# Optimization experiments

Measured on AMD Instinct MI355X. Metric: run time of the kernel, lower is better.

Reference implementation:

```python
import jax, jax.numpy as jnp
import numpy as np

EMBED = 256
HEADS = 8
LEVELS = 3
POINTS = 4
MLP = 4
SS = np.array([[100, 100], [50, 50], [25, 25]], np.int32)  # (H, W) per level


def setup_inputs() -> dict:
    key = jax.random.key(0)
    ks = jax.random.split(key, 12)
    B, Q = 2, 128 * 128
    NV = int((SS[:, 0] * SS[:, 1]).sum())
    C = EMBED
    F = C * MLP
    s = 0.02

    def w(k, shape):
        return jax.random.normal(k, shape, jnp.float32) * s

    return dict(
        query=jax.random.normal(ks[0], (B, Q, C), jnp.float32),
        value=jax.random.normal(ks[1], (B, NV, C), jnp.float32),
        query_pos=jax.random.normal(ks[2], (B, Q, C), jnp.float32),
        ref_pts=jax.random.uniform(ks[3], (B, Q, 2), jnp.float32),
        spatial_shapes=SS,
        level_start_index=np.concatenate([[0], np.cumsum(SS[:, 0] * SS[:, 1])[:-1]]).astype(np.int32),
        ln1_g=jnp.ones(C), ln1_b=jnp.zeros(C),
        ln2_g=jnp.ones(C), ln2_b=jnp.zeros(C),
        W_value=w(ks[4], (C, C)), b_value=jnp.zeros(C),
        W_off=w(ks[5], (C, HEADS * LEVELS * POINTS * 2)), b_off=w(ks[6], (HEADS * LEVELS * POINTS * 2,)),
        W_attn=w(ks[7], (C, HEADS * LEVELS * POINTS)), b_attn=jnp.zeros(HEADS * LEVELS * POINTS),
        W_out=w(ks[8], (C, C)), b_out=jnp.zeros(C),
        W_ffn1=w(ks[9], (C, F)), b_ffn1=jnp.zeros(F),
        W_ffn2=w(ks[10], (F, C)), b_ffn2=jnp.zeros(C),
    )


def _layernorm(x, g, b, eps=1e-5):
    m = x.mean(-1, keepdims=True)
    v = ((x - m) ** 2).mean(-1, keepdims=True)
    return (x - m) * jax.lax.rsqrt(v + eps) * g + b


def _bilinear(v, loc, Hl, Wl):
    # v: [BH, Hl*Wl, d]; loc: [BH, Q, P, 2] normalized to [0,1].
    # grid_sample(align_corners=False, padding=zeros): pixel = loc*size - 0.5
    BH, Q, P, _ = loc.shape
    d = v.shape[-1]
    x = loc[..., 0] * Wl - 0.5
    y = loc[..., 1] * Hl - 0.5
    x0f = jnp.floor(x)
    y0f = jnp.floor(y)
    lx = x - x0f
    ly = y - y0f
    x0 = x0f.astype(jnp.int32)
    y0 = y0f.astype(jnp.int32)

    def gather(xi, yi):
        valid = ((xi >= 0) & (xi < Wl) & (yi >= 0) & (yi < Hl)).astype(v.dtype)
        idx = jnp.clip(yi, 0, Hl - 1) * Wl + jnp.clip(xi, 0, Wl - 1)
        g = jnp.take_along_axis(v, idx.reshape(BH, Q * P, 1), axis=1).reshape(BH, Q, P, d)
        return g * valid[..., None]

    w00 = (1 - lx) * (1 - ly)
    w01 = lx * (1 - ly)
    w10 = (1 - lx) * ly
    w11 = lx * ly
    return (gather(x0, y0) * w00[..., None] + gather(x0 + 1, y0) * w01[..., None]
            + gather(x0, y0 + 1) * w10[..., None] + gather(x0 + 1, y0 + 1) * w11[..., None])


def _forward(query, value, query_pos, ref_pts, spatial_shapes,
             ln1_g, ln1_b, ln2_g, ln2_b,
             W_value, b_value, W_off, b_off, W_attn, b_attn, W_out, b_out,
             W_ffn1, b_ffn1, W_ffn2, b_ffn2):
    B, Q, C = query.shape
    Hh, L, P = HEADS, LEVELS, POINTS
    d = C // Hh
    ss = np.asarray(spatial_shapes)
    starts = np.concatenate([[0], np.cumsum(ss[:, 0] * ss[:, 1])])

    # pre-norm + positional embedding (MSDeformAttn adds query_pos)
    qn = _layernorm(query, ln1_g, ln1_b)
    q = qn + query_pos

    # value projection, split heads
    v = (value @ W_value + b_value).reshape(B, -1, Hh, d)

    off = (q @ W_off + b_off).reshape(B, Q, Hh, L, P, 2)
    aw = jax.nn.softmax((q @ W_attn + b_attn).reshape(B, Q, Hh, L * P), axis=-1)
    aw = aw.reshape(B, Q, Hh, L, P)

    # offset normalizer is (W, H) per level
    normalizer = jnp.asarray(ss[:, ::-1].copy(), jnp.float32)
    # bev_value path: ref_pts broadcast over levels
    loc = ref_pts[:, :, None, None, None, :] + off / normalizer[None, None, None, :, None, :]

    out = jnp.zeros((B * Hh, Q, d), query.dtype)
    for l in range(L):
        Hl, Wl = int(ss[l, 0]), int(ss[l, 1])
        v_l = v[:, starts[l]:starts[l + 1]].transpose(0, 2, 1, 3).reshape(B * Hh, Hl * Wl, d)
        loc_l = loc[:, :, :, l].transpose(0, 2, 1, 3, 4).reshape(B * Hh, Q, P, 2)
        sampled = _bilinear(v_l, loc_l, Hl, Wl)  # [BH, Q, P, d]
        w_l = aw[:, :, :, l].transpose(0, 2, 1, 3).reshape(B * Hh, Q, P)
        out = out + (sampled * w_l[..., None]).sum(2)

    out = out.reshape(B, Hh, Q, d).transpose(0, 2, 1, 3).reshape(B, Q, C)
    x = query + (out @ W_out + b_out)

    h = _layernorm(x, ln2_g, ln2_b)
    x = x + (jax.nn.gelu(h @ W_ffn1 + b_ffn1, approximate=False) @ W_ffn2 + b_ffn2)
    return x


def reference(query, value, query_pos, ref_pts, spatial_shapes, level_start_index,
              ln1_g, ln1_b, ln2_g, ln2_b,
              W_value, b_value, W_off, b_off, W_attn, b_attn, W_out, b_out,
              W_ffn1, b_ffn1, W_ffn2, b_ffn2):
    return _forward(query, value, query_pos, ref_pts, spatial_shapes,
                    ln1_g, ln1_b, ln2_g, ln2_b,
                    W_value, b_value, W_off, b_off, W_attn, b_attn, W_out, b_out,
                    W_ffn1, b_ffn1, W_ffn2, b_ffn2)
```

## Files before the change

### kernel.cpp

```cpp
#include <hip/hip_runtime.h>
#include <hip/hip_bf16.h>

#define BQ      2
#define QLEN    16384
#define CDIM    256
#define HEADS   8
#define LEV     3
#define PTS     4
#define DHEAD   32
#define NVTOT   13125
#define FDIM    1024
#define NTOK    (BQ*QLEN)
#define MROWS_V (BQ*NVTOT)
#define NPROJ   288

typedef __attribute__((ext_vector_type(8))) short short8;
typedef __attribute__((ext_vector_type(4))) float floatx4;

typedef const __attribute__((address_space(1))) unsigned int gu32;
typedef __attribute__((address_space(3))) unsigned int lu32;

struct bf16x4 { __hip_bfloat16 v[4]; };

__device__ __forceinline__ int imin(int a, int b){ return a<b?a:b; }
__device__ __forceinline__ int imax(int a, int b){ return a>b?a:b; }

__device__ __forceinline__ float bf2f(unsigned short u){ return __uint_as_float((unsigned)u << 16); }
__device__ __forceinline__ unsigned short f2bf(float f)
{
    __hip_bfloat16 h = __float2bfloat16(f);
    return *(unsigned short*)&h;
}
__device__ __forceinline__ unsigned long long pack4(float4 v)
{
    unsigned long long r = (unsigned long long)f2bf(v.x)
                         | ((unsigned long long)f2bf(v.y) << 16)
                         | ((unsigned long long)f2bf(v.z) << 32)
                         | ((unsigned long long)f2bf(v.w) << 48);
    return r;
}
__device__ __forceinline__ float4 unpack4(unsigned long long c)
{
    float4 v;
    v.x = bf2f((unsigned short)(c));
    v.y = bf2f((unsigned short)(c >> 16));
    v.z = bf2f((unsigned short)(c >> 32));
    v.w = bf2f((unsigned short)(c >> 48));
    return v;
}

__device__ __forceinline__ float gelu_f(float x)
{
    float u = 0.7978845608028654f * (x + 0.044715f * x * x * x);
    float e = __expf(2.0f * u);
    float th = 1.0f - 2.0f / (e + 1.0f);
    return 0.5f * x * (1.0f + th);
}

__global__ __launch_bounds__(256)
void ln_bf16_k(const float* __restrict__ x, const float* __restrict__ pos,
               const float* __restrict__ g, const float* __restrict__ b,
               __hip_bfloat16* __restrict__ out)
{
    int tok  = blockIdx.x * 4 + (threadIdx.x >> 6);
    int lane = threadIdx.x & 63;
    float4 v = ((const float4*)(x + (size_t)tok * CDIM))[lane];
    float s = v.x + v.y + v.z + v.w;
    #pragma unroll
    for (int o = 32; o > 0; o >>= 1) s += __shfl_down(s, o);
    s = __shfl(s, 0);
    float mean = s * (1.0f / 256.0f);
    float4 c; c.x = v.x - mean; c.y = v.y - mean; c.z = v.z - mean; c.w = v.w - mean;
    float q2 = c.x*c.x + c.y*c.y + c.z*c.z + c.w*c.w;
    #pragma unroll
    for (int o = 32; o > 0; o >>= 1) q2 += __shfl_down(q2, o);
    q2 = __shfl(q2, 0);
    float rstd = rsqrtf(q2 * (1.0f / 256.0f) + 1e-5f);
    float4 gg = ((const float4*)g)[lane];
    float4 bb = ((const float4*)b)[lane];
    float4 o4;
    o4.x = c.x * rstd * gg.x + bb.x;
    o4.y = c.y * rstd * gg.y + bb.y;
    o4.z = c.z * rstd * gg.z + bb.z;
    o4.w = c.w * rstd * gg.w + bb.w;
    if (pos) {
        float4 p = ((const float4*)(pos + (size_t)tok * CDIM))[lane];
        o4.x += p.x; o4.y += p.y; o4.z += p.z; o4.w += p.w;
    }
    *(unsigned long long*)(out + (size_t)tok * CDIM + lane * 4) = pack4(o4);
}

__global__ __launch_bounds__(256)
void cvt_k(const float* __restrict__ in, __hip_bfloat16* __restrict__ out, int n4)
{
    int i = blockIdx.x * 256 + threadIdx.x;
    if (i >= n4) return;
    float4 v = ((const float4*)in)[i];
    *(unsigned long long*)(out + (size_t)i * 4) = pack4(v);
}

__global__ __launch_bounds__(256)
void wt_all_k(const float* __restrict__ Wv,  const float* __restrict__ Woff,
              const float* __restrict__ Wat, const float* __restrict__ Wout,
              const float* __restrict__ W1,  const float* __restrict__ W2,
              const float* __restrict__ boff, const float* __restrict__ bat,
              __hip_bfloat16* __restrict__ o_v,  __hip_bfloat16* __restrict__ o_c,
              __hip_bfloat16* __restrict__ o_out,
              __hip_bfloat16* __restrict__ o_1,  __hip_bfloat16* __restrict__ o_2,
              float* __restrict__ o_bc)
{
    int gid = blockIdx.x * 256 + threadIdx.x;
    if (gid < 65536) {
        int idx = gid, n = idx >> 8, k = idx & 255;
        o_v[idx] = __float2bfloat16(Wv[(size_t)k * 256 + n]);
    } else if (gid < 163840) {
        int idx = gid - 65536, n = idx >> 8, k = idx & 255;
        float v = 0.0f;
        if (n < 192)       v = Woff[(size_t)k * 192 + n];
        else if (n < 288)  v = Wat[(size_t)k * 96 + (n - 192)];
        o_c[idx] = __float2bfloat16(v);
    } else if (gid < 229376) {
        int idx = gid - 163840, n = idx >> 8, k = idx & 255;
        o_out[idx] = __float2bfloat16(Wout[(size_t)k * 256 + n]);
    } else if (gid < 491520) {
        int idx = gid - 229376, n = idx >> 8, k = idx & 255;
        o_1[idx] = __float2bfloat16(W1[(size_t)k * 1024 + n]);
    } else if (gid < 753664) {
        int idx = gid - 491520, n = idx >> 10, k = idx & 1023;
        o_2[idx] = __float2bfloat16(W2[(size_t)k * 256 + n]);
    } else if (gid < 753952) {
        int idx = gid - 753664;
        o_bc[idx] = (idx < 192) ? boff[idx] : bat[idx - 192];
    }
}

enum { EP_PLAIN_BF16 = 0, EP_VSCAT_BF16 = 1, EP_RES = 2, EP_GELU_BF16 = 3 };

__global__ __launch_bounds__(256)
void mm_k(const __hip_bfloat16* __restrict__ A, const __hip_bfloat16* __restrict__ Bt,
          const float* __restrict__ bias, const float* __restrict__ res,
          void* __restrict__ Cout, int M, int N, int K, int mode)
{
    __shared__ float4 smem4[2048];
    __hip_bfloat16* Ws = (__hip_bfloat16*)smem4;
    __hip_bfloat16* Ts = (__hip_bfloat16*)smem4 + 128*64;
    unsigned long long* st = (unsigned long long*)smem4;
    int t = threadIdx.x;
    int lane = t & 63;
    int wave = t >> 6;
    int wm = wave >> 1, wn = wave & 1;
    int lm = lane & 15, lk = lane >> 4;
    int m0 = blockIdx.x * 128;
    int n0 = blockIdx.y * 128;

    floatx4 acc[4][4];
    #pragma unroll
    for (int i = 0; i < 4; i++)
        #pragma unroll
        for (int j = 0; j < 4; j++) acc[i][j] = (floatx4)0.0f;

    for (int kt = 0; kt < K; kt += 64) {
        #pragma unroll
        for (int i = 0; i < 4; i++) {
            int cc  = i * 256 + t;
            int row = cc >> 3;
            int c   = cc & 7;
            int kc  = c ^ (row & 7);
            int ra  = m0 + row; if (ra >= M) ra = M - 1;
            const __hip_bfloat16* gw = Bt + (size_t)(n0 + row) * K + kt + kc * 8;
            const __hip_bfloat16* gt = A  + (size_t)ra * K + kt + kc * 8;
            __builtin_amdgcn_global_load_lds((gu32*)gw, (lu32*)(Ws + cc * 8), 16, 0, 0);
            __builtin_amdgcn_global_load_lds((gu32*)gt, (lu32*)(Ts + cc * 8), 16, 0, 0);
        }
        __syncthreads();
        #pragma unroll
        for (int ks = 0; ks < 2; ks++) {
            short8 wf[4], tf[4];
            #pragma unroll
            for (int i = 0; i < 4; i++) {
                int rw = wn * 64 + i * 16 + lm;
                int cw = (ks * 4 + lk) ^ (rw & 7);
                wf[i] = *(const short8*)(Ws + (rw * 8 + cw) * 8);
                int rt = wm * 64 + i * 16 + lm;
                int ct = (ks * 4 + lk) ^ (rt & 7);
                tf[i] = *(const short8*)(Ts + (rt * 8 + ct) * 8);
            }
            #pragma unroll
            for (int i = 0; i < 4; i++)
                #pragma unroll
                for (int j = 0; j < 4; j++)
                    acc[i][j] = __builtin_amdgcn_mfma_f32_16x16x32_bf16(wf[i], tf[j], acc[i][j], 0, 0, 0);
        }
        __syncthreads();
    }

    #pragma unroll
    for (int i = 0; i < 4; i++) {
        int chan = n0 + wn * 64 + i * 16 + lk * 4;
        float4 b4 = make_float4(0.f, 0.f, 0.f, 0.f);
        if (chan < N) b4 = *(const float4*)(bias + chan);
        int c4 = wn * 16 + i * 4 + lk;
        #pragma unroll
        for (int j = 0; j < 4; j++) {
            int tl = wm * 64 + j * 16 + lm;
            float4 v;
            v.x = acc[i][j][0] + b4.x;
            v.y = acc[i][j][1] + b4.y;
            v.z = acc[i][j][2] + b4.z;
            v.w = acc[i][j][3] + b4.w;
            st[tl * 32 + (c4 ^ (tl & 31))] = pack4(v);
        }
    }
    __syncthreads();

    int rel  = (t & 31) * 4;
    int c4r  = t & 31;
    #pragma unroll
    for (int it = 0; it < 16; it++) {
        int tl   = it * 8 + (t >> 5);
        int tok  = m0 + tl;
        int chan = n0 + rel;
        if (tok >= M || chan >= N) continue;
        unsigned long long chunk = st[tl * 32 + (c4r ^ (tl & 31))];
        if (mode == EP_PLAIN_BF16) {
            *(unsigned long long*)((__hip_bfloat16*)Cout + (size_t)tok * N + chan) = chunk;
        } else if (mode == EP_VSCAT_BF16) {
            int bb  = tok / NVTOT;
            int pix = tok - bb * NVTOT;
            int hd  = chan >> 5, dc = chan & 31;
            *(unsigned long long*)((__hip_bfloat16*)Cout
                + (((size_t)(bb * HEADS + hd)) * NVTOT + pix) * DHEAD + dc) = chunk;
        } else if (mode == EP_GELU_BF16) {
            float4 v = unpack4(chunk);
            v.x = gelu_f(v.x); v.y = gelu_f(v.y); v.z = gelu_f(v.z); v.w = gelu_f(v.w);
            *(unsigned long long*)((__hip_bfloat16*)Cout + (size_t)tok * N + chan) = pack4(v);
        } else {
            float4 v = unpack4(chunk);
            float4 rr = *(const float4*)(res + (size_t)tok * N + chan);
            v.x += rr.x; v.y += rr.y; v.z += rr.z; v.w += rr.w;
            *(float4*)((float*)Cout + (size_t)tok * N + chan) = v;
        }
    }
}

__global__ __launch_bounds__(256)
void sample_k(const __hip_bfloat16* __restrict__ v, const __hip_bfloat16* __restrict__ cbuf,
              const float* __restrict__ ref, __hip_bfloat16* __restrict__ out)
{
    __shared__ int4   metaIdx[4 * 104];
    __shared__ float4 metaW[4 * 104];

    int wid  = threadIdx.x >> 6;
    int lane = threadIdx.x & 63;
    int t    = blockIdx.x * 4 + wid;
    int b    = t >> 14;
    float rx = ref[(size_t)t * 2 + 0];
    float ry = ref[(size_t)t * 2 + 1];
    const __hip_bfloat16* crow = cbuf + (size_t)t * NPROJ;

    #pragma unroll
    for (int rnd = 0; rnd < 2; rnd++) {
        int slot = rnd * 64 + lane;
        int h = slot >> 4, p = slot & 15;
        int pc = imin(p, 11);
        unsigned upk = *(const unsigned*)(crow + h * 24 + pc * 2);
        float ox = bf2f((unsigned short)upk);
        float oy = bf2f((unsigned short)(upk >> 16));
        float logit = bf2f(*(const unsigned short*)(crow + 192 + h * 12 + pc));
        float mx = logit;
        #pragma unroll
        for (int o = 8; o > 0; o >>= 1) mx = fmaxf(mx, __shfl_xor(mx, o, 16));
        float e = (p < 12) ? __expf(logit - mx) : 0.0f;
        float ssum = e;
        #pragma unroll
        for (int o = 8; o > 0; o >>= 1) ssum += __shfl_xor(ssum, o, 16);
        float aw = e / ssum;

        if (p < 12) {
            int l = p >> 2;
            float fS = (l == 0) ? 100.0f : ((l == 1) ? 50.0f : 25.0f);
            int   Wl = (l == 0) ? 100 : ((l == 1) ? 50 : 25);
            int   st = (l == 0) ? 0 : ((l == 1) ? 10000 : 12500);
            float x = (rx + ox / fS) * fS - 0.5f;
            float y = (ry + oy / fS) * fS - 0.5f;
            float x0f = floorf(x), y0f = floorf(y);
            float fx = x - x0f, fy = y - y0f;
            int x0 = (int)x0f, y0 = (int)y0f;
            int x1 = x0 + 1,  y1 = y0 + 1;
            int cx0 = imin(imax(x0, 0), Wl - 1), cx1 = imin(imax(x1, 0), Wl - 1);
            int cy0 = imin(imax(y0, 0), Wl - 1), cy1 = imin(imax(y1, 0), Wl - 1);
            float vx0 = (x0 >= 0 && x0 < Wl) ? 1.0f : 0.0f;
            float vx1 = (x1 >= 0 && x1 < Wl) ? 1.0f : 0.0f;
            float vy0 = (y0 >= 0 && y0 < Wl) ? 1.0f : 0.0f;
            float vy1 = (y1 >= 0 && y1 < Wl) ? 1.0f : 0.0f;
            int s = wid * 104 + h * 13 + p;
            metaIdx[s] = make_int4(st + cy0 * Wl + cx0, st + cy0 * Wl + cx1,
                                   st + cy1 * Wl + cx0, st + cy1 * Wl + cx1);
            metaW[s] = make_float4((1.0f - fx) * (1.0f - fy) * aw * vx0 * vy0,
                                   fx * (1.0f - fy) * aw * vx1 * vy0,
                                   (1.0f - fx) * fy * aw * vx0 * vy1,
                                   fx * fy * aw * vx1 * vy1);
        }
    }
    __syncthreads();

    int h  = lane >> 3;
    int c8 = lane & 7;
    const __hip_bfloat16* vbh = v + ((size_t)(b * HEADS + h)) * NVTOT * DHEAD + c8 * 4;
    float4 acc = {0.0f, 0.0f, 0.0f, 0.0f};
    #pragma unroll
    for (int p = 0; p < 12; p++) {
        int s = wid * 104 + h * 13 + p;
        int4   mi = metaIdx[s];
        float4 mw = metaW[s];
        ushort4 r0 = *(const ushort4*)(vbh + (size_t)mi.x * DHEAD);
        ushort4 r1 = *(const ushort4*)(vbh + (size_t)mi.y * DHEAD);
        ushort4 r2 = *(const ushort4*)(vbh + (size_t)mi.z * DHEAD);
        ushort4 r3 = *(const ushort4*)(vbh + (size_t)mi.w * DHEAD);
        acc.x = fmaf(mw.x, bf2f(r0.x), acc.x);
        acc.y = fmaf(mw.x, bf2f(r0.y), acc.y);
        acc.z = fmaf(mw.x, bf2f(r0.z), acc.z);
        acc.w = fmaf(mw.x, bf2f(r0.w), acc.w);
        acc.x = fmaf(mw.y, bf2f(r1.x), acc.x);
        acc.y = fmaf(mw.y, bf2f(r1.y), acc.y);
        acc.z = fmaf(mw.y, bf2f(r1.z), acc.z);
        acc.w = fmaf(mw.y, bf2f(r1.w), acc.w);
        acc.x = fmaf(mw.z, bf2f(r2.x), acc.x);
        acc.y = fmaf(mw.z, bf2f(r2.y), acc.y);
        acc.z = fmaf(mw.z, bf2f(r2.z), acc.z);
        acc.w = fmaf(mw.z, bf2f(r2.w), acc.w);
        acc.x = fmaf(mw.w, bf2f(r3.x), acc.x);
        acc.y = fmaf(mw.w, bf2f(r3.y), acc.y);
        acc.z = fmaf(mw.w, bf2f(r3.z), acc.z);
        acc.w = fmaf(mw.w, bf2f(r3.w), acc.w);
    }
    *(unsigned long long*)(out + (size_t)t * CDIM + h * DHEAD + c8 * 4) = pack4(acc);
}

extern "C" void kernel_launch(void* const* d_in, const int* in_sizes, int n_in,
                              void* d_out, int out_size, void* d_ws, size_t ws_size,
                              hipStream_t stream)
{
    const float* query = (const float*)d_in[0];
    const float* value = (const float*)d_in[1];
    const float* qpos  = (const float*)d_in[2];
    const float* ref   = (const float*)d_in[3];
    const float* ln1g  = (const float*)d_in[6];
    const float* ln1b  = (const float*)d_in[7];
    const float* ln2g  = (const float*)d_in[8];
    const float* ln2b  = (const float*)d_in[9];
    const float* Wv    = (const float*)d_in[10];
    const float* bv    = (const float*)d_in[11];
    const float* Woff  = (const float*)d_in[12];
    const float* boff  = (const float*)d_in[13];
    const float* Wat   = (const float*)d_in[14];
    const float* bat   = (const float*)d_in[15];
    const float* Wout  = (const float*)d_in[16];
    const float* bout  = (const float*)d_in[17];
    const float* W1    = (const float*)d_in[18];
    const float* b1    = (const float*)d_in[19];
    const float* W2    = (const float*)d_in[20];
    const float* b2    = (const float*)d_in[21];
    float* out = (float*)d_out;
    char*  ws  = (char*)d_ws;

    const size_t MB = 1024 * 1024;
    __hip_bfloat16* Wvt   = (__hip_bfloat16*)(ws + 0);
    __hip_bfloat16* Wct   = (__hip_bfloat16*)(ws + 131072);
    __hip_bfloat16* Woutt = (__hip_bfloat16*)(ws + 327680);
    __hip_bfloat16* W1t   = (__hip_bfloat16*)(ws + 458752);
    __hip_bfloat16* W2t   = (__hip_bfloat16*)(ws + 983040);
    float*          bcomb = (float*)(ws + 1507328);
    __hip_bfloat16* qbf   = (__hip_bfloat16*)(ws + 2  * MB);
    __hip_bfloat16* aoutb = (__hip_bfloat16*)(ws + 19 * MB);
    __hip_bfloat16* vbf   = (__hip_bfloat16*)(ws + 36 * MB);
    __hip_bfloat16* vbuf  = (__hip_bfloat16*)(ws + 50 * MB);
    __hip_bfloat16* cbuf  = (__hip_bfloat16*)(ws + 77 * MB);
    __hip_bfloat16* gbf   = (__hip_bfloat16*)(ws + 100 * MB);
    __hip_bfloat16* hbf   = qbf;

    wt_all_k<<<2946, 256, 0, stream>>>(Wv, Woff, Wat, Wout, W1, W2, boff, bat,
                                       Wvt, Wct, Woutt, W1t, W2t, bcomb);
    cvt_k<<<(MROWS_V * CDIM / 4 + 255) / 256, 256, 0, stream>>>(value, vbf, MROWS_V * CDIM / 4);
    ln_bf16_k<<<NTOK / 4, 256, 0, stream>>>(query, qpos, ln1g, ln1b, qbf);
    mm_k<<<dim3((MROWS_V + 127) / 128, 2), 256, 0, stream>>>(
        vbf, Wvt, bv, nullptr, vbuf, MROWS_V, 256, 256, EP_VSCAT_BF16);
    mm_k<<<dim3(NTOK / 128, 3), 256, 0, stream>>>(
        qbf, Wct, bcomb, nullptr, cbuf, NTOK, NPROJ, 256, EP_PLAIN_BF16);
    sample_k<<<NTOK / 4, 256, 0, stream>>>(vbuf, cbuf, ref, aoutb);
    mm_k<<<dim3(NTOK / 128, 2), 256, 0, stream>>>(
        aoutb, Woutt, bout, query, out, NTOK, 256, 256, EP_RES);
    ln_bf16_k<<<NTOK / 4, 256, 0, stream>>>(out, nullptr, ln2g, ln2b, hbf);
    mm_k<<<dim3(NTOK / 128, 8), 256, 0, stream>>>(
        hbf, W1t, b1, nullptr, gbf, NTOK, FDIM, 256, EP_GELU_BF16);
    mm_k<<<dim3(NTOK / 128, 2), 256, 0, stream>>>(
        gbf, W2t, b2, out, out, NTOK, 256, FDIM, EP_RES);
}
```

Baseline: 367.6 us.

## Fuse prep kernels, keep residual in bf16, token-major value layout, cheaper gelu/sampling math

Merges the weight transpose, value conversion and first layernorm into one launch. The intermediate residual stream is now stored as bf16 instead of fp32 and read back in bf16 by the second layernorm and the final GEMM epilogue. The value projection writes plain token-major output, and the sampler gathers 8-byte chunks using pre-shifted byte offsets. GELU uses a sigmoid-form tanh approximation with a hardware reciprocal, and the sample coordinate math is simplified. Together these cut memory traffic and launches, at the cost of extra bf16 rounding on the residual path.

```diff
diff --git a/kernel.cpp b/kernel.cpp
--- a/kernel.cpp
+++ b/kernel.cpp
@@ -16,12 +16,11 @@
 
 typedef __attribute__((ext_vector_type(8))) short short8;
 typedef __attribute__((ext_vector_type(4))) float floatx4;
+typedef unsigned long long u64;
 
 typedef const __attribute__((address_space(1))) unsigned int gu32;
 typedef __attribute__((address_space(3))) unsigned int lu32;
 
-struct bf16x4 { __hip_bfloat16 v[4]; };
-
 __device__ __forceinline__ int imin(int a, int b){ return a<b?a:b; }
 __device__ __forceinline__ int imax(int a, int b){ return a>b?a:b; }
 
@@ -31,15 +30,12 @@
     __hip_bfloat16 h = __float2bfloat16(f);
     return *(unsigned short*)&h;
 }
-__device__ __forceinline__ unsigned long long pack4(float4 v)
-{
-    unsigned long long r = (unsigned long long)f2bf(v.x)
-                         | ((unsigned long long)f2bf(v.y) << 16)
-                         | ((unsigned long long)f2bf(v.z) << 32)
-                         | ((unsigned long long)f2bf(v.w) << 48);
-    return r;
-}
-__device__ __forceinline__ float4 unpack4(unsigned long long c)
+__device__ __forceinline__ u64 pack4(float4 v)
+{
+    return (u64)f2bf(v.x) | ((u64)f2bf(v.y) << 16)
+         | ((u64)f2bf(v.z) << 32) | ((u64)f2bf(v.w) << 48);
+}
+__device__ __forceinline__ float4 unpack4(u64 c)
 {
     float4 v;
     v.x = bf2f((unsigned short)(c));
@@ -51,20 +47,17 @@
 
 __device__ __forceinline__ float gelu_f(float x)
 {
-    float u = 0.7978845608028654f * (x + 0.044715f * x * x * x);
-    float e = __expf(2.0f * u);
-    float th = 1.0f - 2.0f / (e + 1.0f);
-    return 0.5f * x * (1.0f + th);
-}
-
-__global__ __launch_bounds__(256)
-void ln_bf16_k(const float* __restrict__ x, const float* __restrict__ pos,
-               const float* __restrict__ g, const float* __restrict__ b,
-               __hip_bfloat16* __restrict__ out)
-{
-    int tok  = blockIdx.x * 4 + (threadIdx.x >> 6);
-    int lane = threadIdx.x & 63;
-    float4 v = ((const float4*)(x + (size_t)tok * CDIM))[lane];
+    float u2 = x * x;
+    float a  = x * fmaf(0.0713548163f, u2, 1.5957691216f);
+    float e  = __expf(a);
+    float r  = __builtin_amdgcn_rcpf(e + 1.0f);
+    return fmaf(-x, r, x);
+}
+
+__device__ __forceinline__ void ln_core(float4 v, const float* __restrict__ pos, int tok,
+                                        const float* __restrict__ g, const float* __restrict__ b,
+                                        int lane, __hip_bfloat16* __restrict__ out)
+{
     float s = v.x + v.y + v.z + v.w;
     #pragma unroll
     for (int o = 32; o > 0; o >>= 1) s += __shfl_down(s, o);
@@ -87,64 +80,87 @@
         float4 p = ((const float4*)(pos + (size_t)tok * CDIM))[lane];
         o4.x += p.x; o4.y += p.y; o4.z += p.z; o4.w += p.w;
     }
-    *(unsigned long long*)(out + (size_t)tok * CDIM + lane * 4) = pack4(o4);
-}
+    *(u64*)(out + (size_t)tok * CDIM + lane * 4) = pack4(o4);
+}
+
+#define WT_BLOCKS  2946
+#define CVT_BLOCKS 6563
+#define LN_BLOCKS  8192
 
 __global__ __launch_bounds__(256)
-void cvt_k(const float* __restrict__ in, __hip_bfloat16* __restrict__ out, int n4)
-{
-    int i = blockIdx.x * 256 + threadIdx.x;
-    if (i >= n4) return;
-    float4 v = ((const float4*)in)[i];
-    *(unsigned long long*)(out + (size_t)i * 4) = pack4(v);
+void prep_k(const float* __restrict__ Wv,  const float* __restrict__ Woff,
+            const float* __restrict__ Wat, const float* __restrict__ Wout,
+            const float* __restrict__ W1,  const float* __restrict__ W2,
+            const float* __restrict__ boff, const float* __restrict__ bat,
+            const float* __restrict__ value, const float* __restrict__ query,
+            const float* __restrict__ qpos,  const float* __restrict__ ln1g,
+            const float* __restrict__ ln1b,
+            __hip_bfloat16* __restrict__ o_v,  __hip_bfloat16* __restrict__ o_c,
+            __hip_bfloat16* __restrict__ o_out,
+            __hip_bfloat16* __restrict__ o_1,  __hip_bfloat16* __restrict__ o_2,
+            float* __restrict__ o_bc,
+            __hip_bfloat16* __restrict__ vbf,  __hip_bfloat16* __restrict__ qbf)
+{
+    int bx = blockIdx.x;
+    if (bx < WT_BLOCKS) {
+        int gid = bx * 256 + threadIdx.x;
+        if (gid < 65536) {
+            int idx = gid, n = idx >> 8, k = idx & 255;
+            o_v[idx] = __float2bfloat16(Wv[(size_t)k * 256 + n]);
+        } else if (gid < 163840) {
+            int idx = gid - 65536, n = idx >> 8, k = idx & 255;
+            float v = 0.0f;
+            if (n < 192)       v = Woff[(size_t)k * 192 + n];
+            else if (n < 288)  v = Wat[(size_t)k * 96 + (n - 192)];
+            o_c[idx] = __float2bfloat16(v);
+        } else if (gid < 229376) {
+            int idx = gid - 163840, n = idx >> 8, k = idx & 255;
+            o_out[idx] = __float2bfloat16(Wout[(size_t)k * 256 + n]);
+        } else if (gid < 491520) {
+            int idx = gid - 229376, n = idx >> 8, k = idx & 255;
+            o_1[idx] = __float2bfloat16(W1[(size_t)k * 1024 + n]);
+        } else if (gid < 753664) {
+            int idx = gid - 491520, n = idx >> 10, k = idx & 1023;
+            o_2[idx] = __float2bfloat16(W2[(size_t)k * 256 + n]);
+        } else if (gid < 753952) {
+            int idx = gid - 753664;
+            o_bc[idx] = (idx < 192) ? boff[idx] : bat[idx - 192];
+        }
+    } else if (bx < WT_BLOCKS + CVT_BLOCKS) {
+        int i = (bx - WT_BLOCKS) * 256 + threadIdx.x;
+        if (i < MROWS_V * CDIM / 4) {
+            float4 v = ((const float4*)value)[i];
+            *(u64*)(vbf + (size_t)i * 4) = pack4(v);
+        }
+    } else {
+        int tok  = (bx - WT_BLOCKS - CVT_BLOCKS) * 4 + (threadIdx.x >> 6);
+        int lane = threadIdx.x & 63;
+        float4 v = ((const float4*)(query + (size_t)tok * CDIM))[lane];
+        ln_core(v, qpos, tok, ln1g, ln1b, lane, qbf);
+    }
 }
 
 __global__ __launch_bounds__(256)
-void wt_all_k(const float* __restrict__ Wv,  const float* __restrict__ Woff,
-              const float* __restrict__ Wat, const float* __restrict__ Wout,
-              const float* __restrict__ W1,  const float* __restrict__ W2,
-              const float* __restrict__ boff, const float* __restrict__ bat,
-              __hip_bfloat16* __restrict__ o_v,  __hip_bfloat16* __restrict__ o_c,
-              __hip_bfloat16* __restrict__ o_out,
-              __hip_bfloat16* __restrict__ o_1,  __hip_bfloat16* __restrict__ o_2,
-              float* __restrict__ o_bc)
-{
-    int gid = blockIdx.x * 256 + threadIdx.x;
-    if (gid < 65536) {
-        int idx = gid, n = idx >> 8, k = idx & 255;
-        o_v[idx] = __float2bfloat16(Wv[(size_t)k * 256 + n]);
-    } else if (gid < 163840) {
-        int idx = gid - 65536, n = idx >> 8, k = idx & 255;
-        float v = 0.0f;
-        if (n < 192)       v = Woff[(size_t)k * 192 + n];
-        else if (n < 288)  v = Wat[(size_t)k * 96 + (n - 192)];
-        o_c[idx] = __float2bfloat16(v);
-    } else if (gid < 229376) {
-        int idx = gid - 163840, n = idx >> 8, k = idx & 255;
-        o_out[idx] = __float2bfloat16(Wout[(size_t)k * 256 + n]);
-    } else if (gid < 491520) {
-        int idx = gid - 229376, n = idx >> 8, k = idx & 255;
-        o_1[idx] = __float2bfloat16(W1[(size_t)k * 1024 + n]);
-    } else if (gid < 753664) {
-        int idx = gid - 491520, n = idx >> 10, k = idx & 1023;
-        o_2[idx] = __float2bfloat16(W2[(size_t)k * 256 + n]);
-    } else if (gid < 753952) {
-        int idx = gid - 753664;
-        o_bc[idx] = (idx < 192) ? boff[idx] : bat[idx - 192];
-    }
-}
-
-enum { EP_PLAIN_BF16 = 0, EP_VSCAT_BF16 = 1, EP_RES = 2, EP_GELU_BF16 = 3 };
+void ln2_k(const __hip_bfloat16* __restrict__ x, const float* __restrict__ g,
+           const float* __restrict__ b, __hip_bfloat16* __restrict__ out)
+{
+    int tok  = blockIdx.x * 4 + (threadIdx.x >> 6);
+    int lane = threadIdx.x & 63;
+    float4 v = unpack4(((const u64*)(x + (size_t)tok * CDIM))[lane]);
+    ln_core(v, nullptr, tok, g, b, lane, out);
+}
+
+enum { EP_PLAIN_BF16 = 0, EP_GELU_BF16 = 1, EP_RES_F2BF = 2, EP_RES_BF2F = 3 };
 
 __global__ __launch_bounds__(256)
 void mm_k(const __hip_bfloat16* __restrict__ A, const __hip_bfloat16* __restrict__ Bt,
-          const float* __restrict__ bias, const float* __restrict__ res,
+          const float* __restrict__ bias, const void* __restrict__ res,
           void* __restrict__ Cout, int M, int N, int K, int mode)
 {
     __shared__ float4 smem4[2048];
     __hip_bfloat16* Ws = (__hip_bfloat16*)smem4;
     __hip_bfloat16* Ts = (__hip_bfloat16*)smem4 + 128*64;
-    unsigned long long* st = (unsigned long long*)smem4;
+    u64* st = (u64*)smem4;
     int t = threadIdx.x;
     int lane = t & 63;
     int wave = t >> 6;
@@ -213,30 +229,29 @@
     }
     __syncthreads();
 
-    int rel  = (t & 31) * 4;
-    int c4r  = t & 31;
+    int rel = (t & 31) * 4;
+    int c4r = t & 31;
     #pragma unroll
     for (int it = 0; it < 16; it++) {
         int tl   = it * 8 + (t >> 5);
         int tok  = m0 + tl;
         int chan = n0 + rel;
         if (tok >= M || chan >= N) continue;
-        unsigned long long chunk = st[tl * 32 + (c4r ^ (tl & 31))];
+        u64 chunk = st[tl * 32 + (c4r ^ (tl & 31))];
         if (mode == EP_PLAIN_BF16) {
-            *(unsigned long long*)((__hip_bfloat16*)Cout + (size_t)tok * N + chan) = chunk;
-        } else if (mode == EP_VSCAT_BF16) {
-            int bb  = tok / NVTOT;
-            int pix = tok - bb * NVTOT;
-            int hd  = chan >> 5, dc = chan & 31;
-            *(unsigned long long*)((__hip_bfloat16*)Cout
-                + (((size_t)(bb * HEADS + hd)) * NVTOT + pix) * DHEAD + dc) = chunk;
+            *(u64*)((__hip_bfloat16*)Cout + (size_t)tok * N + chan) = chunk;
         } else if (mode == EP_GELU_BF16) {
             float4 v = unpack4(chunk);
             v.x = gelu_f(v.x); v.y = gelu_f(v.y); v.z = gelu_f(v.z); v.w = gelu_f(v.w);
-            *(unsigned long long*)((__hip_bfloat16*)Cout + (size_t)tok * N + chan) = pack4(v);
+            *(u64*)((__hip_bfloat16*)Cout + (size_t)tok * N + chan) = pack4(v);
+        } else if (mode == EP_RES_F2BF) {
+            float4 v = unpack4(chunk);
+            float4 rr = *(const float4*)((const float*)res + (size_t)tok * N + chan);
+            v.x += rr.x; v.y += rr.y; v.z += rr.z; v.w += rr.w;
+            *(u64*)((__hip_bfloat16*)Cout + (size_t)tok * N + chan) = pack4(v);
         } else {
             float4 v = unpack4(chunk);
-            float4 rr = *(const float4*)(res + (size_t)tok * N + chan);
+            float4 rr = unpack4(*(const u64*)((const __hip_bfloat16*)res + (size_t)tok * N + chan));
             v.x += rr.x; v.y += rr.y; v.z += rr.z; v.w += rr.w;
             *(float4*)((float*)Cout + (size_t)tok * N + chan) = v;
         }
@@ -274,15 +289,15 @@
         float ssum = e;
         #pragma unroll
         for (int o = 8; o > 0; o >>= 1) ssum += __shfl_xor(ssum, o, 16);
-        float aw = e / ssum;
+        float aw = e * __builtin_amdgcn_rcpf(ssum);
 
         if (p < 12) {
             int l = p >> 2;
             float fS = (l == 0) ? 100.0f : ((l == 1) ? 50.0f : 25.0f);
             int   Wl = (l == 0) ? 100 : ((l == 1) ? 50 : 25);
             int   st = (l == 0) ? 0 : ((l == 1) ? 10000 : 12500);
-            float x = (rx + ox / fS) * fS - 0.5f;
-            float y = (ry + oy / fS) * fS - 0.5f;
+            float x = fmaf(rx, fS, ox) - 0.5f;
+            float y = fmaf(ry, fS, oy) - 0.5f;
             float x0f = floorf(x), y0f = floorf(y);
             float fx = x - x0f, fy = y - y0f;
             int x0 = (int)x0f, y0 = (int)y0f;
@@ -294,8 +309,8 @@
             float vy0 = (y0 >= 0 && y0 < Wl) ? 1.0f : 0.0f;
             float vy1 = (y1 >= 0 && y1 < Wl) ? 1.0f : 0.0f;
             int s = wid * 104 + h * 13 + p;
-            metaIdx[s] = make_int4(st + cy0 * Wl + cx0, st + cy0 * Wl + cx1,
-                                   st + cy1 * Wl + cx0, st + cy1 * Wl + cx1);
+            metaIdx[s] = make_int4((st + cy0 * Wl + cx0) << 9, (st + cy0 * Wl + cx1) << 9,
+                                   (st + cy1 * Wl + cx0) << 9, (st + cy1 * Wl + cx1) << 9);
             metaW[s] = make_float4((1.0f - fx) * (1.0f - fy) * aw * vx0 * vy0,
                                    fx * (1.0f - fy) * aw * vx1 * vy0,
                                    (1.0f - fx) * fy * aw * vx0 * vy1,
@@ -305,36 +320,49 @@
     __syncthreads();
 
     int h  = lane >> 3;
-    int c8 = lane & 7;
-    const __hip_bfloat16* vbh = v + ((size_t)(b * HEADS + h)) * NVTOT * DHEAD + c8 * 4;
+    int bs = __builtin_amdgcn_readfirstlane(b);
+    const char* vb = (const char*)(v + (size_t)bs * NVTOT * CDIM);
+    int hoff = lane * 8;
     float4 acc = {0.0f, 0.0f, 0.0f, 0.0f};
     #pragma unroll
     for (int p = 0; p < 12; p++) {
         int s = wid * 104 + h * 13 + p;
         int4   mi = metaIdx[s];
         float4 mw = metaW[s];
-        ushort4 r0 = *(const ushort4*)(vbh + (size_t)mi.x * DHEAD);
-        ushort4 r1 = *(const ushort4*)(vbh + (size_t)mi.y * DHEAD);
-        ushort4 r2 = *(const ushort4*)(vbh + (size_t)mi.z * DHEAD);
-        ushort4 r3 = *(const ushort4*)(vbh + (size_t)mi.w * DHEAD);
-        acc.x = fmaf(mw.x, bf2f(r0.x), acc.x);
-        acc.y = fmaf(mw.x, bf2f(r0.y), acc.y);
-        acc.z = fmaf(mw.x, bf2f(r0.z), acc.z);
-        acc.w = fmaf(mw.x, bf2f(r0.w), acc.w);
-        acc.x = fmaf(mw.y, bf2f(r1.x), acc.x);
-        acc.y = fmaf(mw.y, bf2f(r1.y), acc.y);
-        acc.z = fmaf(mw.y, bf2f(r1.z), acc.z);
-        acc.w = fmaf(mw.y, bf2f(r1.w), acc.w);
-        acc.x = fmaf(mw.z, bf2f(r2.x), acc.x);
-        acc.y = fmaf(mw.z, bf2f(r2.y), acc.y);
-        acc.z = fmaf(mw.z, bf2f(r2.z), acc.z);
-        acc.w = fmaf(mw.z, bf2f(r2.w), acc.w);
-        acc.x = fmaf(mw.w, bf2f(r3.x), acc.x);
-        acc.y = fmaf(mw.w, bf2f(r3.y), acc.y);
-        acc.z = fmaf(mw.w, bf2f(r3.z), acc.z);
-        acc.w = fmaf(mw.w, bf2f(r3.w), acc.w);
-    }
-    *(unsigned long long*)(out + (size_t)t * CDIM + h * DHEAD + c8 * 4) = pack4(acc);
+        u64 g0 = *(const u64*)(vb + (unsigned)(mi.x + hoff));
+        u64 g1 = *(const u64*)(vb + (unsigned)(mi.y + hoff));
+        u64 g2 = *(const u64*)(vb + (unsigned)(mi.z + hoff));
+        u64 g3 = *(const u64*)(vb + (unsigned)(mi.w + hoff));
+        {
+            unsigned d0 = (unsigned)g0, d1 = (unsigned)(g0 >> 32);
+            acc.x = fmaf(mw.x, __uint_as_float(d0 << 16), acc.x);
+            acc.y = fmaf(mw.x, __uint_as_float(d0 & 0xffff0000u), acc.y);
+            acc.z = fmaf(mw.x, __uint_as_float(d1 << 16), acc.z);
+            acc.w = fmaf(mw.x, __uint_as_float(d1 & 0xffff0000u), acc.w);
+        }
+        {
+            unsigned d0 = (unsigned)g1, d1 = (unsigned)(g1 >> 32);
+            acc.x = fmaf(mw.y, __uint_as_float(d0 << 16), acc.x);
+            acc.y = fmaf(mw.y, __uint_as_float(d0 & 0xffff0000u), acc.y);
+            acc.z = fmaf(mw.y, __uint_as_float(d1 << 16), acc.z);
+            acc.w = fmaf(mw.y, __uint_as_float(d1 & 0xffff0000u), acc.w);
+        }
+        {
+            unsigned d0 = (unsigned)g2, d1 = (unsigned)(g2 >> 32);
+            acc.x = fmaf(mw.z, __uint_as_float(d0 << 16), acc.x);
+            acc.y = fmaf(mw.z, __uint_as_float(d0 & 0xffff0000u), acc.y);
+            acc.z = fmaf(mw.z, __uint_as_float(d1 << 16), acc.z);
+            acc.w = fmaf(mw.z, __uint_as_float(d1 & 0xffff0000u), acc.w);
+        }
+        {
+            unsigned d0 = (unsigned)g3, d1 = (unsigned)(g3 >> 32);
+            acc.x = fmaf(mw.w, __uint_as_float(d0 << 16), acc.x);
+            acc.y = fmaf(mw.w, __uint_as_float(d0 & 0xffff0000u), acc.y);
+            acc.z = fmaf(mw.w, __uint_as_float(d1 << 16), acc.z);
+            acc.w = fmaf(mw.w, __uint_as_float(d1 & 0xffff0000u), acc.w);
+        }
+    }
+    *(u64*)(out + (size_t)t * CDIM + lane * 4) = pack4(acc);
 }
 
 extern "C" void kernel_launch(void* const* d_in, const int* in_sizes, int n_in,
@@ -375,24 +403,24 @@
     __hip_bfloat16* aoutb = (__hip_bfloat16*)(ws + 19 * MB);
     __hip_bfloat16* vbf   = (__hip_bfloat16*)(ws + 36 * MB);
     __hip_bfloat16* vbuf  = (__hip_bfloat16*)(ws + 50 * MB);
-    __hip_bfloat16* cbuf  = (__hip_bfloat16*)(ws + 77 * MB);
+    __hip_bfloat16* xbf   = (__hip_bfloat16*)(ws + 64 * MB);
+    __hip_bfloat16* cbuf  = (__hip_bfloat16*)(ws + 81 * MB);
     __hip_bfloat16* gbf   = (__hip_bfloat16*)(ws + 100 * MB);
     __hip_bfloat16* hbf   = qbf;
 
-    wt_all_k<<<2946, 256, 0, stream>>>(Wv, Woff, Wat, Wout, W1, W2, boff, bat,
-                                       Wvt, Wct, Woutt, W1t, W2t, bcomb);
-    cvt_k<<<(MROWS_V * CDIM / 4 + 255) / 256, 256, 0, stream>>>(value, vbf, MROWS_V * CDIM / 4);
-    ln_bf16_k<<<NTOK / 4, 256, 0, stream>>>(query, qpos, ln1g, ln1b, qbf);
+    prep_k<<<WT_BLOCKS + CVT_BLOCKS + LN_BLOCKS, 256, 0, stream>>>(
+        Wv, Woff, Wat, Wout, W1, W2, boff, bat, value, query, qpos, ln1g, ln1b,
+        Wvt, Wct, Woutt, W1t, W2t, bcomb, vbf, qbf);
     mm_k<<<dim3((MROWS_V + 127) / 128, 2), 256, 0, stream>>>(
-        vbf, Wvt, bv, nullptr, vbuf, MROWS_V, 256, 256, EP_VSCAT_BF16);
+        vbf, Wvt, bv, nullptr, vbuf, MROWS_V, 256, 256, EP_PLAIN_BF16);
     mm_k<<<dim3(NTOK / 128, 3), 256, 0, stream>>>(
         qbf, Wct, bcomb, nullptr, cbuf, NTOK, NPROJ, 256, EP_PLAIN_BF16);
     sample_k<<<NTOK / 4, 256, 0, stream>>>(vbuf, cbuf, ref, aoutb);
     mm_k<<<dim3(NTOK / 128, 2), 256, 0, stream>>>(
-        aoutb, Woutt, bout, query, out, NTOK, 256, 256, EP_RES);
-    ln_bf16_k<<<NTOK / 4, 256, 0, stream>>>(out, nullptr, ln2g, ln2b, hbf);
+        aoutb, Woutt, bout, query, xbf, NTOK, 256, 256, EP_RES_F2BF);
+    ln2_k<<<NTOK / 4, 256, 0, stream>>>(xbf, ln2g, ln2b, hbf);
     mm_k<<<dim3(NTOK / 128, 8), 256, 0, stream>>>(
         hbf, W1t, b1, nullptr, gbf, NTOK, FDIM, 256, EP_GELU_BF16);
     mm_k<<<dim3(NTOK / 128, 2), 256, 0, stream>>>(
-        gbf, W2t, b2, out, out, NTOK, 256, FDIM, EP_RES);
-}
+        gbf, W2t, b2, xbf, out, NTOK, 256, 1024, EP_RES_BF2F);
+}
```

Result: faster. 347.8 us (-5.4%).
